# Optimization experiments

Measured on AMD Instinct MI355X. Metric: run time of the kernel, lower is better.

The kernel has to match this reference:

```python
import jax, jax.numpy as jnp
import numpy as np

EPS = 1e-5      # BatchNorm eps (eval mode, running stats at init: mean=0, var=1)
SLOPE = 0.2     # LeakyReLU negative slope


def _knn_idx(x, k):
    # x: (B, N, D) -> (B, N, k) indices of k nearest neighbors (squared L2, feature space)
    sq = jnp.sum(x * x, axis=-1)                              # (B, N)
    dist = sq[:, :, None] + sq[:, None, :] - 2.0 * jnp.einsum('bnd,bmd->bnm', x, x)
    return jax.lax.top_k(-dist, k)[1]                         # nearest = largest of -dist


def _bn_lrelu(y, gamma, beta):
    # eval BatchNorm with running_mean=0, running_var=1, then LeakyReLU(0.2)
    y = y * (gamma / jnp.sqrt(1.0 + EPS)) + beta
    return jnp.where(y >= 0, y, SLOPE * y)


def _edge_conv(x, W, gamma, beta, k):
    # x: (B, N, D); W: (C_out, 2D). Returns (B, N, C_out) after max over k neighbors.
    idx = _knn_idx(x, k)                                      # (B, N, k)
    nb = jax.vmap(lambda xt, i: xt[i])(x, idx)                # (B, N, k, D) neighbor gather
    ctr = jnp.broadcast_to(x[:, :, None, :], nb.shape)
    feat = jnp.concatenate([nb - ctr, ctr], axis=-1)          # (B, N, k, 2D)
    y = jnp.einsum('bnkd,od->bnko', feat, W)                  # 1x1 conv (no bias)
    y = _bn_lrelu(y, gamma, beta)
    return jnp.max(y, axis=2)                                 # max-pool over neighbors


def setup_inputs() -> dict:
    key = jax.random.key(0)
    ks = jax.random.split(key, 16)
    B, N, k, out_dim = 8, 4096, 20, 512
    x = jax.random.normal(ks[0], (B, 3, N), dtype=jnp.float32)
    dims = [(64, 6), (64, 128), (128, 128), (256, 256), (out_dim, 512)]
    inp = {'x': x, 'k': k}
    for i, (co, ci) in enumerate(dims, start=1):
        inp[f'W{i}'] = jax.random.normal(ks[3 * i - 2], (co, ci), dtype=jnp.float32) * (1.0 / np.sqrt(ci))
        inp[f'g{i}'] = jax.random.uniform(ks[3 * i - 1], (co,), dtype=jnp.float32, minval=0.5, maxval=1.5)
        inp[f'b{i}'] = 0.1 * jax.random.normal(ks[3 * i], (co,), dtype=jnp.float32)
    return inp


def reference(x, W1, g1, b1, W2, g2, b2, W3, g3, b3, W4, g4, b4, W5, g5, b5, k):
    xt = jnp.transpose(x, (0, 2, 1))                          # (B, N, 3)
    x1 = _edge_conv(xt, W1, g1, b1, k)                        # (B, N, 64)
    x2 = _edge_conv(x1, W2, g2, b2, k)                        # (B, N, 64)
    x3 = _edge_conv(x2, W3, g3, b3, k)                        # (B, N, 128)
    x4 = _edge_conv(x3, W4, g4, b4, k)                        # (B, N, 256)
    h = jnp.concatenate([x1, x2, x3, x4], axis=-1)            # (B, N, 512)
    y = _bn_lrelu(jnp.einsum('bnd,od->bno', h, W5), g5, b5)   # (B, N, out_dim)
    return jnp.concatenate([jnp.max(y, axis=1), jnp.mean(y, axis=1)], axis=-1)  # (B, 2*out_dim)
```

## Files before the change

kernel.cpp:

```cpp
#include <hip/hip_runtime.h>
#include <math.h>

#define BATCH 8
#define N_PTS 4096
#define KNN 20
#define EPS_BN 1e-5f
#define SLOPE 0.2f
#define M_ROWS (BATCH * N_PTS)

typedef __attribute__((ext_vector_type(8))) short short8;
typedef __attribute__((ext_vector_type(4))) float float4v;
typedef __attribute__((ext_vector_type(16))) float float16v;

__device__ __forceinline__ unsigned short f2bf(float f) {
    unsigned u = __float_as_uint(f);
    unsigned r = (u + 0x7FFFu + ((u >> 16) & 1u)) >> 16;
    return (unsigned short)r;
}
__device__ __forceinline__ float bf2f(unsigned short h) {
    return __uint_as_float((unsigned)h << 16);
}

__global__ void convert_x1(const float* __restrict__ x,
                           unsigned short* __restrict__ xh, unsigned short* __restrict__ xl,
                           float* __restrict__ sq) {
    int i = blockIdx.x * blockDim.x + threadIdx.x;
    if (i >= M_ROWS) return;
    int b = i / N_PTS, n = i % N_PTS;
    float v[3], s = 0.f;
    #pragma unroll
    for (int d = 0; d < 3; ++d) {
        v[d] = x[((size_t)b * 3 + d) * N_PTS + n];
        s += v[d] * v[d];
    }
    sq[i] = s;
    #pragma unroll
    for (int d = 0; d < 32; ++d) {
        float f = (d < 3) ? v[d] : 0.f;
        unsigned short h = f2bf(f);
        xh[(size_t)i * 32 + d] = h;
        xl[(size_t)i * 32 + d] = f2bf(f - bf2f(h));
    }
}

__global__ void sqnorm_hl(const unsigned short* __restrict__ hh,
                          const unsigned short* __restrict__ hl,
                          int D, float* __restrict__ sq) {
    int w = threadIdx.x >> 6, lane = threadIdx.x & 63;
    int row = blockIdx.x * 4 + w;
    if (row >= M_ROWS) return;
    const unsigned short* ph = hh + (size_t)row * 512;
    const unsigned short* pl = hl + (size_t)row * 512;
    float s = 0.f;
    for (int d = lane; d < D; d += 64) {
        float v = bf2f(ph[d]) + bf2f(pl[d]);
        s += v * v;
    }
    #pragma unroll
    for (int off = 32; off > 0; off >>= 1) s += __shfl_down(s, off, 64);
    if (lane == 0) sq[row] = s;
}

__global__ void repack_edge_split(const float* __restrict__ W, int Co, int D, int KP,
                                  unsigned short* __restrict__ Wh, unsigned short* __restrict__ Wl) {
    int i = blockIdx.x * blockDim.x + threadIdx.x;
    int tot = 2 * Co * KP;
    if (i >= tot) return;
    int r = i / KP, d = i % KP;
    float v = 0.f;
    if (d < D) v = (r < Co) ? W[(size_t)r * 2 * D + d] : W[(size_t)(r - Co) * 2 * D + D + d];
    unsigned short h = f2bf(v);
    Wh[i] = h; Wl[i] = f2bf(v - bf2f(h));
}

__global__ void repack_w5_split(const float* __restrict__ W,
                                unsigned short* __restrict__ Wh, unsigned short* __restrict__ Wl) {
    int i = blockIdx.x * blockDim.x + threadIdx.x;
    if (i >= 512 * 512) return;
    float v = W[i];
    unsigned short h = f2bf(v);
    Wh[i] = h; Wl[i] = f2bf(v - bf2f(h));
}

template<int DPAD>
__launch_bounds__(256, 2)
__global__ void knn_mfma(const unsigned short* __restrict__ Xh,
                         const unsigned short* __restrict__ Xl,
                         int strideX,
                         const float* __restrict__ sq, int* __restrict__ idxout) {
    constexpr int KS16 = DPAD / 16;
    constexpr int C8   = DPAD / 8;
    constexpr int XK   = (C8 - 1) < 7 ? (C8 - 1) : 7;
    constexpr int SB   = 64 * DPAD;
    constexpr size_t STAGE = (size_t)2 * SB * 2 + (size_t)64 * 65 * 4 + 64 * 4;
    constexpr size_t MERGE = (size_t)64 * 61 * 4 * 2;
    constexpr size_t POOL  = STAGE > MERGE ? STAGE : MERGE;
    __shared__ __align__(16) char smem[POOL];
    unsigned short* BhS = (unsigned short*)smem;
    unsigned short* BlS = BhS + SB;
    float* Sf  = (float*)(smem + (size_t)2 * SB * 2);
    float* sqs = Sf + 64 * 65;
    float*    kb = (float*)smem;
    unsigned* ib = (unsigned*)(kb + 64 * 61);

    const int b = blockIdx.y;
    const int row0 = blockIdx.x * 64;
    const int tid = threadIdx.x;
    const int w = tid >> 6, lane = tid & 63;
    const int l31 = lane & 31, lh = lane >> 5;
    const int r = tid & 63, t = tid >> 6;
    const int rbase = (w & 1) * 32;
    const int cb32  = (w >> 1) * 32;

    const unsigned short* Xhb = Xh + (size_t)b * N_PTS * strideX;
    const unsigned short* Xlb = Xl + (size_t)b * N_PTS * strideX;
    const float* sqb = sq + (size_t)b * N_PTS;

    short8 ah[KS16], al[KS16];
    #pragma unroll
    for (int ks = 0; ks < KS16; ++ks) {
        size_t o = (size_t)(row0 + rbase + l31) * strideX + ks * 16 + lh * 8;
        ah[ks] = *(const short8*)(Xhb + o);
        al[ks] = *(const short8*)(Xlb + o);
    }

    float fv[KNN]; int fi[KNN];
    #pragma unroll
    for (int p = 0; p < KNN; ++p) { fv[p] = INFINITY; fi[p] = 0x7FFFFFFF; }

    for (int c0 = 0; c0 < N_PTS; c0 += 64) {
        __syncthreads();
        #pragma unroll
        for (int it = 0; it < (64 * C8 + 255) / 256; ++it) {
            int tt = tid + it * 256;
            int col = tt / C8, kcs = tt % C8;
            int kcg = kcs ^ (col & XK);
            size_t o = (size_t)(c0 + col) * strideX + kcg * 8;
            *(short8*)&BhS[tt * 8] = *(const short8*)(Xhb + o);
            *(short8*)&BlS[tt * 8] = *(const short8*)(Xlb + o);
        }
        if (tid < 64) sqs[tid] = sqb[c0 + tid];
        __syncthreads();

        float16v acc = {};

        const int colL = cb32 + l31;
        const int cbase_us = colL * DPAD;
        #pragma unroll
        for (int ks = 0; ks < KS16; ++ks) {
            int ch = ((ks * 2 + lh) ^ (colL & XK)) * 8;
            short8 bh = *(const short8*)&BhS[cbase_us + ch];
            short8 bl = *(const short8*)&BlS[cbase_us + ch];
            acc = __builtin_amdgcn_mfma_f32_32x32x16_bf16(ah[ks], bh, acc, 0, 0, 0);
            acc = __builtin_amdgcn_mfma_f32_32x32x16_bf16(al[ks], bh, acc, 0, 0, 0);
            acc = __builtin_amdgcn_mfma_f32_32x32x16_bf16(ah[ks], bl, acc, 0, 0, 0);
        }

        {
            float sc = sqs[colL];
            int pos = (colL & 3) * 16 + (colL >> 2);
            #pragma unroll
            for (int reg = 0; reg < 16; ++reg) {
                int rowL = rbase + (reg & 3) + 8 * (reg >> 2) + 4 * lh;
                Sf[rowL * 65 + pos] = sc - 2.f * acc[reg];
            }
        }
        __syncthreads();

        const int sbase = r * 65 + t * 16;
        unsigned mask = 0;
        #pragma unroll
        for (int jj = 0; jj < 16; ++jj) {
            float v = Sf[sbase + jj];
            if (v < fv[KNN - 1]) mask |= (1u << jj);
        }
        while (mask) {
            int jj = __ffs(mask) - 1;
            mask &= mask - 1;
            float v = Sf[sbase + jj];
            if (v < fv[KNN - 1]) {
                fv[KNN - 1] = v;
                fi[KNN - 1] = c0 + (jj << 2) + t;
                #pragma unroll
                for (int p = KNN - 1; p > 0; --p) {
                    float va = fv[p - 1], vb = fv[p];
                    int   ia = fi[p - 1], ic = fi[p];
                    bool sw = vb < va;
                    fv[p - 1] = sw ? vb : va; fv[p] = sw ? va : vb;
                    fi[p - 1] = sw ? ic : ia; fi[p] = sw ? ia : ic;
                }
            }
        }
    }
    __syncthreads();

    if (t > 0) {
        #pragma unroll
        for (int p = 0; p < KNN; ++p) {
            kb[r * 61 + (t - 1) * KNN + p] = fv[p];
            ib[r * 61 + (t - 1) * KNN + p] = (unsigned)fi[p];
        }
    }
    __syncthreads();
    if (tid < 64) {
        #pragma unroll 1
        for (int qq = 0; qq < 3 * KNN; ++qq) {
            float    v  = kb[tid * 61 + qq];
            unsigned ii = ib[tid * 61 + qq];
            bool ins = (v < fv[KNN - 1]) ||
                       (v == fv[KNN - 1] && (int)ii < fi[KNN - 1]);
            if (ins) {
                fv[KNN - 1] = v; fi[KNN - 1] = (int)ii;
                #pragma unroll
                for (int p = KNN - 1; p > 0; --p) {
                    float va = fv[p - 1], vb = fv[p];
                    int   ia = fi[p - 1], ic = fi[p];
                    bool sw = (vb < va) || (vb == va && ic < ia);
                    fv[p - 1] = sw ? vb : va; fv[p] = sw ? va : vb;
                    fi[p - 1] = sw ? ic : ia; fi[p] = sw ? ia : ic;
                }
            }
        }
        int* op = idxout + ((size_t)(b * N_PTS + row0 + tid)) * KNN;
        #pragma unroll
        for (int p = 0; p < KNN; ++p) op[p] = fi[p];
    }
}

__launch_bounds__(256)
__global__ void fgemm(const unsigned short* __restrict__ Ah, const unsigned short* __restrict__ Al,
                      int strideA, int K,
                      const unsigned short* __restrict__ Wh, const unsigned short* __restrict__ Wl,
                      int C, float* __restrict__ out, int fuse_bn,
                      const float* __restrict__ g, const float* __restrict__ beta) {
    __shared__ unsigned short AhS[128 * 40];
    __shared__ unsigned short AlS[128 * 40];
    __shared__ unsigned short BhS[128 * 40];
    __shared__ unsigned short BlS[128 * 40];

    const int c0 = blockIdx.x * 128;
    const int m0 = blockIdx.y * 128;
    const int tid = threadIdx.x;
    const int w = tid >> 6, lane = tid & 63;
    const int n = lane & 15, q = lane >> 4;

    float4v acc[2][8];
    #pragma unroll
    for (int rt = 0; rt < 2; ++rt)
        #pragma unroll
        for (int ct = 0; ct < 8; ++ct) acc[rt][ct] = (float4v){0.f, 0.f, 0.f, 0.f};

    for (int kk = 0; kk < K; kk += 32) {
        __syncthreads();
        for (int tt = tid; tt < 512; tt += 256) {
            int rr = tt >> 2, c8 = tt & 3;
            size_t oa = (size_t)(m0 + rr) * strideA + kk + c8 * 8;
            *(short8*)&AhS[rr * 40 + c8 * 8] = *(const short8*)(Ah + oa);
            *(short8*)&AlS[rr * 40 + c8 * 8] = *(const short8*)(Al + oa);
            size_t ob = (size_t)(c0 + rr) * K + kk + c8 * 8;
            *(short8*)&BhS[rr * 40 + c8 * 8] = *(const short8*)(Wh + ob);
            *(short8*)&BlS[rr * 40 + c8 * 8] = *(const short8*)(Wl + ob);
        }
        __syncthreads();

        short8 af[2][2];
        #pragma unroll
        for (int rt = 0; rt < 2; ++rt) {
            af[rt][0] = *(const short8*)&AhS[(w * 32 + rt * 16 + n) * 40 + q * 8];
            af[rt][1] = *(const short8*)&AlS[(w * 32 + rt * 16 + n) * 40 + q * 8];
        }
        #pragma unroll
        for (int ct = 0; ct < 8; ++ct) {
            short8 bh = *(const short8*)&BhS[(ct * 16 + n) * 40 + q * 8];
            short8 bl = *(const short8*)&BlS[(ct * 16 + n) * 40 + q * 8];
            #pragma unroll
            for (int rt = 0; rt < 2; ++rt) {
                acc[rt][ct] = __builtin_amdgcn_mfma_f32_16x16x32_bf16(af[rt][0], bh, acc[rt][ct], 0, 0, 0);
                acc[rt][ct] = __builtin_amdgcn_mfma_f32_16x16x32_bf16(af[rt][1], bh, acc[rt][ct], 0, 0, 0);
                acc[rt][ct] = __builtin_amdgcn_mfma_f32_16x16x32_bf16(af[rt][0], bl, acc[rt][ct], 0, 0, 0);
            }
        }
    }

    #pragma unroll
    for (int rt = 0; rt < 2; ++rt)
        #pragma unroll
        for (int ct = 0; ct < 8; ++ct) {
            int c = c0 + ct * 16 + n;
            float sc = 1.f, bt = 0.f;
            if (fuse_bn) { sc = g[c] / sqrtf(1.f + EPS_BN); bt = beta[c]; }
            #pragma unroll
            for (int e = 0; e < 4; ++e) {
                int m = m0 + w * 32 + rt * 16 + q * 4 + e;
                float v = acc[rt][ct][e];
                if (fuse_bn) { v = v * sc + bt; v = (v >= 0.f) ? v : SLOPE * v; }
                out[(size_t)m * C + c] = v;
            }
        }
}

__global__ void pool_kernel(const float* __restrict__ zc2, int Co,
                            const int* __restrict__ idx,
                            const float* __restrict__ g, const float* __restrict__ beta,
                            unsigned short* __restrict__ hh, unsigned short* __restrict__ hl,
                            int hoff) {
    int n = blockIdx.x, b = blockIdx.y;
    int o = threadIdx.x;
    size_t bn = (size_t)b * N_PTS + n;
    const int* ip = idx + bn * KNN;
    float zn   = zc2[bn * (size_t)(2 * Co) + o];
    float base = zc2[bn * (size_t)(2 * Co) + Co + o] - zn;
    float m = -INFINITY;
    #pragma unroll
    for (int j = 0; j < KNN; ++j) {
        size_t rr = (size_t)b * N_PTS + ip[j];
        m = fmaxf(m, zc2[rr * (size_t)(2 * Co) + o]);
    }
    float y = m + base;
    float sc = g[o] / sqrtf(1.f + EPS_BN);
    y = y * sc + beta[o];
    y = (y >= 0.f) ? y : SLOPE * y;
    unsigned short h = f2bf(y);
    hh[bn * 512 + hoff + o] = h;
    hl[bn * 512 + hoff + o] = f2bf(y - bf2f(h));
}

__global__ void reduce_partial(const float* __restrict__ y5,
                               float* __restrict__ pmax, float* __restrict__ psum) {
    int chunk = blockIdx.x, b = blockIdx.y, c = threadIdx.x;
    float mx = -INFINITY, sm = 0.f;
    for (int qq = 0; qq < 128; ++qq) {
        int n = chunk * 128 + qq;
        float v = y5[((size_t)b * N_PTS + n) * 512 + c];
        mx = fmaxf(mx, v);
        sm += v;
    }
    pmax[((size_t)b * 32 + chunk) * 512 + c] = mx;
    psum[((size_t)b * 32 + chunk) * 512 + c] = sm;
}

__global__ void reduce_final(const float* __restrict__ pmax,
                             const float* __restrict__ psum,
                             float* __restrict__ out) {
    int i = blockIdx.x * blockDim.x + threadIdx.x;
    if (i >= BATCH * 512) return;
    int b = i / 512, c = i % 512;
    float mx = -INFINITY, sm = 0.f;
    for (int qq = 0; qq < 32; ++qq) {
        mx = fmaxf(mx, pmax[((size_t)b * 32 + qq) * 512 + c]);
        sm += psum[((size_t)b * 32 + qq) * 512 + c];
    }
    out[(size_t)b * 1024 + c] = mx;
    out[(size_t)b * 1024 + 512 + c] = sm * (1.f / 4096.f);
}

extern "C" void kernel_launch(void* const* d_in, const int* in_sizes, int n_in,
                              void* d_out, int out_size, void* d_ws, size_t ws_size,
                              hipStream_t stream) {
    const float* x = (const float*)d_in[0];
    const float* W[5], *gg[5], *bb[5];
    for (int i = 0; i < 5; ++i) {
        W[i]  = (const float*)d_in[2 + 3 * i];
        gg[i] = (const float*)d_in[3 + 3 * i];
        bb[i] = (const float*)d_in[4 + 3 * i];
    }
    float* outp = (float*)d_out;

    char* wsb = (char*)d_ws;
    size_t off = 0;
    unsigned short* x1h = (unsigned short*)(wsb + off); off += (size_t)M_ROWS * 32 * 2;
    unsigned short* x1l = (unsigned short*)(wsb + off); off += (size_t)M_ROWS * 32 * 2;
    float* sq = (float*)(wsb + off); off += (size_t)M_ROWS * 4;
    int*   idx = (int*)(wsb + off); off += (size_t)M_ROWS * KNN * 4;
    unsigned short* Wh = (unsigned short*)(wsb + off); off += (size_t)512 * 512 * 2;
    unsigned short* Wl = (unsigned short*)(wsb + off); off += (size_t)512 * 512 * 2;
    unsigned short* hh = (unsigned short*)(wsb + off); off += (size_t)M_ROWS * 512 * 2;
    unsigned short* hl = (unsigned short*)(wsb + off); off += (size_t)M_ROWS * 512 * 2;
    float* zc2 = (float*)(wsb + off); off += (size_t)M_ROWS * 512 * 4;
    float* pmx = (float*)(wsb + off); off += (size_t)BATCH * 32 * 512 * 4;
    float* psm = (float*)(wsb + off); off += (size_t)BATCH * 32 * 512 * 4;
    (void)ws_size; (void)in_sizes; (void)n_in; (void)out_size;

    convert_x1<<<(M_ROWS + 255) / 256, 256, 0, stream>>>(x, x1h, x1l, sq);

    struct L { int D, Co, KP, hoff; };
    const L layers[4] = { {3, 64, 32, 0}, {64, 64, 64, 64}, {64, 128, 64, 128}, {128, 256, 128, 256} };

    for (int li = 0; li < 4; ++li) {
        const L& ly = layers[li];
        const unsigned short* Ahp;
        const unsigned short* Alp;
        int strideA;
        if (li == 0) { Ahp = x1h; Alp = x1l; strideA = 32; }
        else {
            int po = layers[li - 1].hoff;
            Ahp = hh + po; Alp = hl + po; strideA = 512;
            sqnorm_hl<<<M_ROWS / 4, 256, 0, stream>>>(Ahp, Alp, ly.D, sq);
        }

        if (li == 0)
            knn_mfma<32><<<dim3(N_PTS / 64, BATCH), 256, 0, stream>>>(Ahp, Alp, strideA, sq, idx);
        else if (ly.D == 64)
            knn_mfma<64><<<dim3(N_PTS / 64, BATCH), 256, 0, stream>>>(Ahp, Alp, strideA, sq, idx);
        else
            knn_mfma<128><<<dim3(N_PTS / 64, BATCH), 256, 0, stream>>>(Ahp, Alp, strideA, sq, idx);

        repack_edge_split<<<(2 * ly.Co * ly.KP + 255) / 256, 256, 0, stream>>>(
            W[li], ly.Co, ly.D, ly.KP, Wh, Wl);
        fgemm<<<dim3((2 * ly.Co) / 128, M_ROWS / 128), 256, 0, stream>>>(
            Ahp, Alp, strideA, ly.KP, Wh, Wl, 2 * ly.Co, zc2, 0, nullptr, nullptr);
        pool_kernel<<<dim3(N_PTS, BATCH), ly.Co, 0, stream>>>(
            zc2, ly.Co, idx, gg[li], bb[li], hh, hl, ly.hoff);
    }

    repack_w5_split<<<(512 * 512 + 255) / 256, 256, 0, stream>>>(W[4], Wh, Wl);
    fgemm<<<dim3(4, M_ROWS / 128), 256, 0, stream>>>(
        hh, hl, 512, 512, Wh, Wl, 512, zc2, 1, gg[4], bb[4]);

    reduce_partial<<<dim3(32, BATCH), 512, 0, stream>>>(zc2, pmx, psm);
    reduce_final<<<(BATCH * 512 + 255) / 256, 256, 0, stream>>>(pmx, psm, outp);
}
```

Measured before the change: 1.460 ms.

## Prefetch next KNN tile into registers and prune candidates with shared thresholds

Restructures the KNN column loop so the next 64-column tile and its squared norms are loaded from global memory into registers while the current tile's top-k selection runs. The registers are written into shared memory afterwards, which removes one barrier per iteration. It also publishes each thread's current 20th-best distance in shared memory. Each row's candidates are then filtered against the minimum of the four per-row thresholds, which cuts wasted insertion work. The cost is more register pressure from the prefetch buffers and a little extra shared memory. The NIT calculation no longer rounds up, so small padded dims could load incorrectly.

```diff
diff --git a/kernel.cpp b/kernel.cpp
--- a/kernel.cpp
+++ b/kernel.cpp
@@ -92,7 +92,8 @@
     constexpr int C8   = DPAD / 8;
     constexpr int XK   = (C8 - 1) < 7 ? (C8 - 1) : 7;
     constexpr int SB   = 64 * DPAD;
-    constexpr size_t STAGE = (size_t)2 * SB * 2 + (size_t)64 * 65 * 4 + 64 * 4;
+    constexpr int NIT  = (64 * C8) / 256;
+    constexpr size_t STAGE = (size_t)2 * SB * 2 + (size_t)64 * 65 * 4 + 64 * 4 + 256 * 4;
     constexpr size_t MERGE = (size_t)64 * 61 * 4 * 2;
     constexpr size_t POOL  = STAGE > MERGE ? STAGE : MERGE;
     __shared__ __align__(16) char smem[POOL];
@@ -100,6 +101,7 @@
     unsigned short* BlS = BhS + SB;
     float* Sf  = (float*)(smem + (size_t)2 * SB * 2);
     float* sqs = Sf + 64 * 65;
+    float* thrT = sqs + 64;
     float*    kb = (float*)smem;
     unsigned* ib = (unsigned*)(kb + 64 * 61);
 
@@ -128,18 +130,19 @@
     #pragma unroll
     for (int p = 0; p < KNN; ++p) { fv[p] = INFINITY; fi[p] = 0x7FFFFFFF; }
 
+    #pragma unroll
+    for (int it = 0; it < NIT; ++it) {
+        int tt = tid + it * 256;
+        int col = tt / C8, kcs = tt % C8;
+        int kcg = kcs ^ (col & XK);
+        size_t o = (size_t)col * strideX + kcg * 8;
+        *(short8*)&BhS[tt * 8] = *(const short8*)(Xhb + o);
+        *(short8*)&BlS[tt * 8] = *(const short8*)(Xlb + o);
+    }
+    if (tid < 64) sqs[tid] = sqb[tid];
+    thrT[tid] = INFINITY;
+
     for (int c0 = 0; c0 < N_PTS; c0 += 64) {
-        __syncthreads();
-        #pragma unroll
-        for (int it = 0; it < (64 * C8 + 255) / 256; ++it) {
-            int tt = tid + it * 256;
-            int col = tt / C8, kcs = tt % C8;
-            int kcg = kcs ^ (col & XK);
-            size_t o = (size_t)(c0 + col) * strideX + kcg * 8;
-            *(short8*)&BhS[tt * 8] = *(const short8*)(Xhb + o);
-            *(short8*)&BlS[tt * 8] = *(const short8*)(Xlb + o);
-        }
-        if (tid < 64) sqs[tid] = sqb[c0 + tid];
         __syncthreads();
 
         float16v acc = {};
@@ -167,12 +170,34 @@
         }
         __syncthreads();
 
+        const int c1 = c0 + 64;
+        short8 sh[NIT], sl[NIT];
+        float sqv = 0.f;
+        if (c1 < N_PTS) {
+            #pragma unroll
+            for (int it = 0; it < NIT; ++it) {
+                int tt = tid + it * 256;
+                int col = tt / C8, kcs = tt % C8;
+                int kcg = kcs ^ (col & XK);
+                size_t o = (size_t)(c1 + col) * strideX + kcg * 8;
+                sh[it] = *(const short8*)(Xhb + o);
+                sl[it] = *(const short8*)(Xlb + o);
+            }
+            if (tid < 64) sqv = sqb[c1 + tid];
+        }
+
+        float fT = fminf(fminf(thrT[r], thrT[64 + r]),
+                         fminf(thrT[128 + r], thrT[192 + r]));
+
         const int sbase = r * 65 + t * 16;
         unsigned mask = 0;
-        #pragma unroll
-        for (int jj = 0; jj < 16; ++jj) {
-            float v = Sf[sbase + jj];
-            if (v < fv[KNN - 1]) mask |= (1u << jj);
+        {
+            float f19 = fv[KNN - 1];
+            #pragma unroll
+            for (int jj = 0; jj < 16; ++jj) {
+                float v = Sf[sbase + jj];
+                if (v < f19 && v <= fT) mask |= (1u << jj);
+            }
         }
         while (mask) {
             int jj = __ffs(mask) - 1;
@@ -191,6 +216,18 @@
                 }
             }
         }
+
+        if (c1 < N_PTS) {
+            #pragma unroll
+            for (int it = 0; it < NIT; ++it) {
+                int tt = tid + it * 256;
+                *(short8*)&BhS[tt * 8] = sh[it];
+                *(short8*)&BlS[tt * 8] = sl[it];
+            }
+            if (tid < 64) sqs[tid] = sqv;
+        }
+
+        thrT[t * 64 + r] = fv[KNN - 1];
     }
     __syncthreads();
 
```

New measurement: 1.543 ms. 1.06x slower.

## Split KNN column range across blocks, share per-row thresholds, merge partial top-k

Applied to the files above, without the earlier changes.

The KNN kernel now splits the candidate columns into two halves via a third grid dimension, doubling the number of blocks, and writes per-half sorted top-k lists that a new merge kernel combines. Within a block, the four threads handling one row share their current 20th-best distance through shared memory, and candidates are pruned against the minimum of those thresholds, so fewer go through insertion sorting. The score tile load is vectorized with a padded stride of 66 and a wider swizzle mask. This adds an extra kernel launch and global traffic for the partial lists, and the shared-threshold pruning must stay exact so that neighbor selection is unchanged.

```diff
diff --git a/kernel.cpp b/kernel.cpp
--- a/kernel.cpp
+++ b/kernel.cpp
@@ -7,8 +7,11 @@
 #define EPS_BN 1e-5f
 #define SLOPE 0.2f
 #define M_ROWS (BATCH * N_PTS)
+#define NSPLIT 2
+#define CHALF (N_PTS / NSPLIT)
 
 typedef __attribute__((ext_vector_type(8))) short short8;
+typedef __attribute__((ext_vector_type(2))) float float2v;
 typedef __attribute__((ext_vector_type(4))) float float4v;
 typedef __attribute__((ext_vector_type(16))) float float16v;
 
@@ -87,24 +90,29 @@
 __global__ void knn_mfma(const unsigned short* __restrict__ Xh,
                          const unsigned short* __restrict__ Xl,
                          int strideX,
-                         const float* __restrict__ sq, int* __restrict__ idxout) {
+                         const float* __restrict__ sq,
+                         float* __restrict__ pv, int* __restrict__ pi) {
     constexpr int KS16 = DPAD / 16;
     constexpr int C8   = DPAD / 8;
-    constexpr int XK   = (C8 - 1) < 7 ? (C8 - 1) : 7;
+    constexpr int XK   = (C8 - 1) < 15 ? (C8 - 1) : 15;
     constexpr int SB   = 64 * DPAD;
-    constexpr size_t STAGE = (size_t)2 * SB * 2 + (size_t)64 * 65 * 4 + 64 * 4;
+    constexpr int NIT  = (64 * C8) / 256;
+    constexpr size_t STAGE = (size_t)2 * SB * 2 + (size_t)64 * 66 * 4 + 64 * 4 + 256 * 4;
     constexpr size_t MERGE = (size_t)64 * 61 * 4 * 2;
     constexpr size_t POOL  = STAGE > MERGE ? STAGE : MERGE;
     __shared__ __align__(16) char smem[POOL];
     unsigned short* BhS = (unsigned short*)smem;
     unsigned short* BlS = BhS + SB;
     float* Sf  = (float*)(smem + (size_t)2 * SB * 2);
-    float* sqs = Sf + 64 * 65;
+    float* sqs = Sf + 64 * 66;
+    float* thrT = sqs + 64;
     float*    kb = (float*)smem;
     unsigned* ib = (unsigned*)(kb + 64 * 61);
 
     const int b = blockIdx.y;
     const int row0 = blockIdx.x * 64;
+    const int sidx = blockIdx.z;
+    const int cs0 = sidx * CHALF;
     const int tid = threadIdx.x;
     const int w = tid >> 6, lane = tid & 63;
     const int l31 = lane & 31, lh = lane >> 5;
@@ -127,11 +135,12 @@
     float fv[KNN]; int fi[KNN];
     #pragma unroll
     for (int p = 0; p < KNN; ++p) { fv[p] = INFINITY; fi[p] = 0x7FFFFFFF; }
-
-    for (int c0 = 0; c0 < N_PTS; c0 += 64) {
+    thrT[tid] = INFINITY;
+
+    for (int c0 = cs0; c0 < cs0 + CHALF; c0 += 64) {
         __syncthreads();
         #pragma unroll
-        for (int it = 0; it < (64 * C8 + 255) / 256; ++it) {
+        for (int it = 0; it < NIT; ++it) {
             int tt = tid + it * 256;
             int col = tt / C8, kcs = tt % C8;
             int kcg = kcs ^ (col & XK);
@@ -162,17 +171,26 @@
             #pragma unroll
             for (int reg = 0; reg < 16; ++reg) {
                 int rowL = rbase + (reg & 3) + 8 * (reg >> 2) + 4 * lh;
-                Sf[rowL * 65 + pos] = sc - 2.f * acc[reg];
+                Sf[rowL * 66 + pos] = sc - 2.f * acc[reg];
             }
         }
         __syncthreads();
 
-        const int sbase = r * 65 + t * 16;
+        float fT = fminf(fminf(thrT[r], thrT[64 + r]),
+                         fminf(thrT[128 + r], thrT[192 + r]));
+
+        const int sbase = r * 66 + t * 16;
         unsigned mask = 0;
-        #pragma unroll
-        for (int jj = 0; jj < 16; ++jj) {
-            float v = Sf[sbase + jj];
-            if (v < fv[KNN - 1]) mask |= (1u << jj);
+        {
+            float f19 = fv[KNN - 1];
+            float2v c2[8];
+            #pragma unroll
+            for (int u = 0; u < 8; ++u) c2[u] = *(const float2v*)&Sf[sbase + 2 * u];
+            #pragma unroll
+            for (int u = 0; u < 8; ++u) {
+                if (c2[u][0] < f19 && c2[u][0] <= fT) mask |= (1u << (2 * u));
+                if (c2[u][1] < f19 && c2[u][1] <= fT) mask |= (1u << (2 * u + 1));
+            }
         }
         while (mask) {
             int jj = __ffs(mask) - 1;
@@ -191,6 +209,8 @@
                 }
             }
         }
+
+        thrT[t * 64 + r] = fv[KNN - 1];
     }
     __syncthreads();
 
@@ -221,9 +241,32 @@
                 }
             }
         }
-        int* op = idxout + ((size_t)(b * N_PTS + row0 + tid)) * KNN;
-        #pragma unroll
-        for (int p = 0; p < KNN; ++p) op[p] = fi[p];
+        size_t pb = ((size_t)(b * N_PTS + row0 + tid) * NSPLIT + sidx) * KNN;
+        #pragma unroll
+        for (int p = 0; p < KNN; ++p) { pv[pb + p] = fv[p]; pi[pb + p] = fi[p]; }
+    }
+}
+
+__global__ void knn_merge(const float* __restrict__ pv, const int* __restrict__ pi,
+                          int* __restrict__ idxout) {
+    int row = blockIdx.x * blockDim.x + threadIdx.x;
+    if (row >= M_ROWS) return;
+    const float* va = pv + (size_t)row * NSPLIT * KNN;
+    const float* vb = va + KNN;
+    const int*   ja = pi + (size_t)row * NSPLIT * KNN;
+    const int*   jb = ja + KNN;
+    int* op = idxout + (size_t)row * KNN;
+    int a = 0, bq = 0;
+    #pragma unroll 1
+    for (int p = 0; p < KNN; ++p) {
+        bool av = a < KNN, bv = bq < KNN;
+        float fa = av ? va[a] : INFINITY;
+        float fb = bv ? vb[bq] : INFINITY;
+        int   ia = av ? ja[a] : 0x7FFFFFFF;
+        int   ibx = bv ? jb[bq] : 0x7FFFFFFF;
+        bool takeA = av && (!bv || fa < fb || (fa == fb && ia < ibx));
+        op[p] = takeA ? ia : ibx;
+        if (takeA) ++a; else ++bq;
     }
 }
 
@@ -379,6 +422,8 @@
     float* zc2 = (float*)(wsb + off); off += (size_t)M_ROWS * 512 * 4;
     float* pmx = (float*)(wsb + off); off += (size_t)BATCH * 32 * 512 * 4;
     float* psm = (float*)(wsb + off); off += (size_t)BATCH * 32 * 512 * 4;
+    float* pv  = (float*)(wsb + off); off += (size_t)M_ROWS * NSPLIT * KNN * 4;
+    int*   pi  = (int*)(wsb + off);   off += (size_t)M_ROWS * NSPLIT * KNN * 4;
     (void)ws_size; (void)in_sizes; (void)n_in; (void)out_size;
 
     convert_x1<<<(M_ROWS + 255) / 256, 256, 0, stream>>>(x, x1h, x1l, sq);
@@ -399,11 +444,12 @@
         }
 
         if (li == 0)
-            knn_mfma<32><<<dim3(N_PTS / 64, BATCH), 256, 0, stream>>>(Ahp, Alp, strideA, sq, idx);
+            knn_mfma<32><<<dim3(N_PTS / 64, BATCH, NSPLIT), 256, 0, stream>>>(Ahp, Alp, strideA, sq, pv, pi);
         else if (ly.D == 64)
-            knn_mfma<64><<<dim3(N_PTS / 64, BATCH), 256, 0, stream>>>(Ahp, Alp, strideA, sq, idx);
+            knn_mfma<64><<<dim3(N_PTS / 64, BATCH, NSPLIT), 256, 0, stream>>>(Ahp, Alp, strideA, sq, pv, pi);
         else
-            knn_mfma<128><<<dim3(N_PTS / 64, BATCH), 256, 0, stream>>>(Ahp, Alp, strideA, sq, idx);
+            knn_mfma<128><<<dim3(N_PTS / 64, BATCH, NSPLIT), 256, 0, stream>>>(Ahp, Alp, strideA, sq, pv, pi);
+        knn_merge<<<(M_ROWS + 255) / 256, 256, 0, stream>>>(pv, pi, idx);
 
         repack_edge_split<<<(2 * ly.Co * ly.KP + 255) / 256, 256, 0, stream>>>(
             W[li], ly.Co, ly.D, ly.KP, Wh, Wl);
```

Result: slower. 1.696 ms (+16.1%).

## Make kNN tiles warp-local: direct global B loads, per-wave scoring, no block barriers

Applied to the files above, without the earlier changes.

The kNN kernel no longer stages each 64-column candidate tile in shared memory behind block-wide barriers. Each wave loads its own B fragments straight from global memory, writes its 32x32 distance tile to a private shared-memory slice, and filters rows within the wave. The ownership of partial top-k lists changes so each lane owns a row and 16 columns. A cross-half shuffle tightens the insertion threshold. For small feature dimensions the three split-bf16 MFMAs use independent accumulators to shorten the dependency chain. The final merge now reads four partial lists per row. This trades shared-memory reuse for more global/L2 traffic, since each wave reloads the B tile instead of sharing it. It also relies on an explicit lgkmcnt wait instead of a barrier for intra-wave LDS visibility.

```diff
diff --git a/kernel.cpp b/kernel.cpp
--- a/kernel.cpp
+++ b/kernel.cpp
@@ -89,26 +89,18 @@
                          int strideX,
                          const float* __restrict__ sq, int* __restrict__ idxout) {
     constexpr int KS16 = DPAD / 16;
-    constexpr int C8   = DPAD / 8;
-    constexpr int XK   = (C8 - 1) < 7 ? (C8 - 1) : 7;
-    constexpr int SB   = 64 * DPAD;
-    constexpr size_t STAGE = (size_t)2 * SB * 2 + (size_t)64 * 65 * 4 + 64 * 4;
-    constexpr size_t MERGE = (size_t)64 * 61 * 4 * 2;
-    constexpr size_t POOL  = STAGE > MERGE ? STAGE : MERGE;
+    constexpr int SST  = 33;
+    constexpr size_t POOL = (size_t)64 * 4 * KNN * 4 * 2;
     __shared__ __align__(16) char smem[POOL];
-    unsigned short* BhS = (unsigned short*)smem;
-    unsigned short* BlS = BhS + SB;
-    float* Sf  = (float*)(smem + (size_t)2 * SB * 2);
-    float* sqs = Sf + 64 * 65;
+    float* Sfw = (float*)smem + (size_t)(threadIdx.x >> 6) * 32 * SST;
     float*    kb = (float*)smem;
-    unsigned* ib = (unsigned*)(kb + 64 * 61);
+    unsigned* ib = (unsigned*)(kb + 64 * 4 * KNN);
 
     const int b = blockIdx.y;
     const int row0 = blockIdx.x * 64;
     const int tid = threadIdx.x;
     const int w = tid >> 6, lane = tid & 63;
     const int l31 = lane & 31, lh = lane >> 5;
-    const int r = tid & 63, t = tid >> 6;
     const int rbase = (w & 1) * 32;
     const int cb32  = (w >> 1) * 32;
 
@@ -124,63 +116,62 @@
         al[ks] = *(const short8*)(Xlb + o);
     }
 
+    const unsigned short* pBh = Xhb + (size_t)(cb32 + l31) * strideX + lh * 8;
+    const unsigned short* pBl = Xlb + (size_t)(cb32 + l31) * strideX + lh * 8;
+    const float* psq = sqb + cb32 + l31;
+
     float fv[KNN]; int fi[KNN];
     #pragma unroll
     for (int p = 0; p < KNN; ++p) { fv[p] = INFINITY; fi[p] = 0x7FFFFFFF; }
 
     for (int c0 = 0; c0 < N_PTS; c0 += 64) {
-        __syncthreads();
-        #pragma unroll
-        for (int it = 0; it < (64 * C8 + 255) / 256; ++it) {
-            int tt = tid + it * 256;
-            int col = tt / C8, kcs = tt % C8;
-            int kcg = kcs ^ (col & XK);
-            size_t o = (size_t)(c0 + col) * strideX + kcg * 8;
-            *(short8*)&BhS[tt * 8] = *(const short8*)(Xhb + o);
-            *(short8*)&BlS[tt * 8] = *(const short8*)(Xlb + o);
-        }
-        if (tid < 64) sqs[tid] = sqb[c0 + tid];
-        __syncthreads();
-
-        float16v acc = {};
-
-        const int colL = cb32 + l31;
-        const int cbase_us = colL * DPAD;
+        short8 bh[KS16], bl[KS16];
         #pragma unroll
         for (int ks = 0; ks < KS16; ++ks) {
-            int ch = ((ks * 2 + lh) ^ (colL & XK)) * 8;
-            short8 bh = *(const short8*)&BhS[cbase_us + ch];
-            short8 bl = *(const short8*)&BlS[cbase_us + ch];
-            acc = __builtin_amdgcn_mfma_f32_32x32x16_bf16(ah[ks], bh, acc, 0, 0, 0);
-            acc = __builtin_amdgcn_mfma_f32_32x32x16_bf16(al[ks], bh, acc, 0, 0, 0);
-            acc = __builtin_amdgcn_mfma_f32_32x32x16_bf16(ah[ks], bl, acc, 0, 0, 0);
-        }
-
-        {
-            float sc = sqs[colL];
-            int pos = (colL & 3) * 16 + (colL >> 2);
-            #pragma unroll
-            for (int reg = 0; reg < 16; ++reg) {
-                int rowL = rbase + (reg & 3) + 8 * (reg >> 2) + 4 * lh;
-                Sf[rowL * 65 + pos] = sc - 2.f * acc[reg];
+            bh[ks] = *(const short8*)(pBh + (size_t)c0 * strideX + ks * 16);
+            bl[ks] = *(const short8*)(pBl + (size_t)c0 * strideX + ks * 16);
+        }
+        float sc = psq[c0];
+
+        float16v a0 = {}, a1 = {}, a2 = {};
+        #pragma unroll
+        for (int ks = 0; ks < KS16; ++ks) {
+            if (KS16 <= 4) {
+                a0 = __builtin_amdgcn_mfma_f32_32x32x16_bf16(ah[ks], bh[ks], a0, 0, 0, 0);
+                a1 = __builtin_amdgcn_mfma_f32_32x32x16_bf16(al[ks], bh[ks], a1, 0, 0, 0);
+                a2 = __builtin_amdgcn_mfma_f32_32x32x16_bf16(ah[ks], bl[ks], a2, 0, 0, 0);
+            } else {
+                a0 = __builtin_amdgcn_mfma_f32_32x32x16_bf16(ah[ks], bh[ks], a0, 0, 0, 0);
+                a0 = __builtin_amdgcn_mfma_f32_32x32x16_bf16(al[ks], bh[ks], a0, 0, 0, 0);
+                a0 = __builtin_amdgcn_mfma_f32_32x32x16_bf16(ah[ks], bl[ks], a0, 0, 0, 0);
             }
         }
-        __syncthreads();
-
-        const int sbase = r * 65 + t * 16;
+
+        #pragma unroll
+        for (int reg = 0; reg < 16; ++reg) {
+            int rowL = (reg & 3) + 8 * (reg >> 2) + 4 * lh;
+            float v = (KS16 <= 4) ? (a0[reg] + a1[reg] + a2[reg]) : a0[reg];
+            Sfw[rowL * SST + l31] = sc - 2.f * v;
+        }
+        asm volatile("s_waitcnt lgkmcnt(0)" ::: "memory");
+
+        float f19 = fv[KNN - 1];
+        float fT = fminf(f19, __shfl_xor(f19, 32, 64));
+
+        const int sbase = l31 * SST + lh * 16;
         unsigned mask = 0;
         #pragma unroll
         for (int jj = 0; jj < 16; ++jj) {
-            float v = Sf[sbase + jj];
-            if (v < fv[KNN - 1]) mask |= (1u << jj);
+            float v = Sfw[sbase + jj];
+            if (v < f19 && v <= fT) mask |= (1u << jj);
         }
         while (mask) {
             int jj = __ffs(mask) - 1;
             mask &= mask - 1;
-            float v = Sf[sbase + jj];
+            float v = Sfw[sbase + jj];
             if (v < fv[KNN - 1]) {
                 fv[KNN - 1] = v;
-                fi[KNN - 1] = c0 + (jj << 2) + t;
+                fi[KNN - 1] = c0 + cb32 + lh * 16 + jj;
                 #pragma unroll
                 for (int p = KNN - 1; p > 0; --p) {
                     float va = fv[p - 1], vb = fv[p];
@@ -192,21 +183,24 @@
             }
         }
     }
+
     __syncthreads();
-
-    if (t > 0) {
-        #pragma unroll
-        for (int p = 0; p < KNN; ++p) {
-            kb[r * 61 + (t - 1) * KNN + p] = fv[p];
-            ib[r * 61 + (t - 1) * KNN + p] = (unsigned)fi[p];
-        }
+    {
+        int rowb = rbase + l31;
+        int slot = (w >> 1) * 2 + lh;
+        int base = (rowb * 4 + slot) * KNN;
+        #pragma unroll
+        for (int p = 0; p < KNN; ++p) { kb[base + p] = fv[p]; ib[base + p] = (unsigned)fi[p]; }
     }
     __syncthreads();
     if (tid < 64) {
+        int base = tid * 4 * KNN;
+        #pragma unroll
+        for (int p = 0; p < KNN; ++p) { fv[p] = kb[base + p]; fi[p] = (int)ib[base + p]; }
         #pragma unroll 1
         for (int qq = 0; qq < 3 * KNN; ++qq) {
-            float    v  = kb[tid * 61 + qq];
-            unsigned ii = ib[tid * 61 + qq];
+            float    v  = kb[base + KNN + qq];
+            unsigned ii = ib[base + KNN + qq];
             bool ins = (v < fv[KNN - 1]) ||
                        (v == fv[KNN - 1] && (int)ii < fi[KNN - 1]);
             if (ins) {
```

New measurement: 1.474 ms. Within noise of the previous version (+0.9%).
